# Performance work log

Hardware: AMD Instinct MI355X
Metric: run time of the kernel (lower is better)

Reference implementation:

```python
import jax, jax.numpy as jnp
import numpy as np

B, T, P, D = 8, 512, 2048, 768
TOKEN_HALF = 0.15
PATCH_HALF = 0.03  # small patch boxes


def _make_boxes(key, b, n, half):
    c = jax.random.uniform(key, (b, n, 2), dtype=jnp.float32)
    lo = jnp.clip(c - half, 0.0, 1.0)
    hi = jnp.clip(c + half, 0.0, 1.0)
    return jnp.concatenate([lo, hi], axis=-1)  # (b, n, 4): x0,y0,x1,y1


def setup_inputs() -> dict:
    key = jax.random.key(0)
    k1, k2, k3, k4 = jax.random.split(key, 4)
    patch_feats = jax.random.normal(k1, (B, P, D), dtype=jnp.float32)
    token_boxes = _make_boxes(k2, B, T, TOKEN_HALF)
    patch_boxes = _make_boxes(k3, B, P, PATCH_HALF)
    token_mask = jnp.ones((B, T), dtype=bool)
    scorer_w = jax.random.normal(k4, (D,), dtype=jnp.float32) * 0.02
    scorer_b = jnp.zeros((1,), dtype=jnp.float32)
    return {"patch_feats": patch_feats, "token_boxes": token_boxes,
            "patch_boxes": patch_boxes, "token_mask": token_mask,
            "scorer_w": scorer_w, "scorer_b": scorer_b}


def _patches_in_token_boxes(patch_boxes, tb):
    # patch center containment test: (B,T,P) bool
    cx = 0.5 * (patch_boxes[..., 0] + patch_boxes[..., 2])  # (B,P)
    cy = 0.5 * (patch_boxes[..., 1] + patch_boxes[..., 3])  # (B,P)
    cx = cx[:, None, :]
    cy = cy[:, None, :]
    return ((cx >= tb[..., 0:1]) & (cx <= tb[..., 2:3]) &
            (cy >= tb[..., 1:2]) & (cy <= tb[..., 3:4]))


def reference(patch_feats, token_boxes, patch_boxes, token_mask, scorer_w, scorer_b):
    # normalize token boxes if given in 0..1000 coords (data-dependent, via where)
    tb = token_boxes
    scale = jnp.where(tb.max() > 1.5, jnp.float32(1.0 / 1000.0), jnp.float32(1.0))
    tb = tb * scale

    in_box = _patches_in_token_boxes(patch_boxes, tb)          # (B,T,P)
    in_box = in_box & token_mask[:, :, None]
    region_mask = jnp.any(in_box, axis=-1)                      # (B,T)

    scores = patch_feats @ scorer_w + scorer_b[0]               # (B,P)
    scores = jnp.broadcast_to(scores[:, None, :], in_box.shape)  # (B,T,P)
    scores = jnp.where(in_box, scores, jnp.float32(-10000.0))
    attn = jax.nn.softmax(scores, axis=-1)                      # (B,T,P)

    region_feats = jnp.einsum('btp,bpd->btd', attn, patch_feats)
    region_feats = region_feats * region_mask[..., None].astype(region_feats.dtype)
    return region_feats, region_mask
```

## Files before the change

### kernel.cpp

```cpp
#include <hip/hip_runtime.h>

#define B 8
#define T 512
#define P 2048
#define D 768
#define KDIM P
#define NSPLIT 2
#define KSPLIT (KDIM / NSPLIT)

typedef unsigned short ushort_t;
using short8 = __attribute__((ext_vector_type(8))) short;
using f32x4v = __attribute__((ext_vector_type(4))) float;

#define IDX_SCALE 0
#define IDX_SCORES 64
#define IDX_SCORES2 (64 + B*P)
#define IDX_CX (64 + B*P)
#define IDX_CY (64 + 2*B*P)
#define OFF_ATTN_BYTES 197120
#define OFF_FT_BYTES (OFF_ATTN_BYTES + (size_t)B*T*P*2)
#define OFF_PART_BYTES (OFF_FT_BYTES + (size_t)B*D*P*2)
#define WS_NEED (OFF_PART_BYTES + (size_t)NSPLIT*B*T*D*2)

#define GLD16(gsrc, ldst) \
    __builtin_amdgcn_global_load_lds((const __attribute__((address_space(1))) void*)(gsrc), \
                                     (__attribute__((address_space(3))) void*)(ldst), 16, 0, 0)

#define SCHED_FENCE() __builtin_amdgcn_sched_barrier(0)
#define RAW_BARRIER() do { SCHED_FENCE(); __builtin_amdgcn_s_barrier(); SCHED_FENCE(); } while (0)

__device__ inline ushort_t f2bf(float x) {
    union { float f; unsigned u; } v; v.f = x;
    unsigned r = v.u + 0x7fffu + ((v.u >> 16) & 1u);
    return (ushort_t)(r >> 16);
}

__global__ void k_scale(const float* __restrict__ tboxes, float* __restrict__ ws) {
    __shared__ float red[4];
    int tid = threadIdx.x;
    float m = -1e30f;
    const float4* tb4 = (const float4*)tboxes;
    #pragma unroll
    for (int i = 0; i < 16; ++i) {
        float4 v = tb4[tid + i * 256];
        m = fmaxf(fmaxf(fmaxf(m, v.x), fmaxf(v.y, v.z)), v.w);
    }
    #pragma unroll
    for (int off = 1; off < 64; off <<= 1) m = fmaxf(m, __shfl_xor(m, off));
    if ((tid & 63) == 0) red[tid >> 6] = m;
    __syncthreads();
    if (tid == 0) {
        float mb = fmaxf(fmaxf(red[0], red[1]), fmaxf(red[2], red[3]));
        ws[IDX_SCALE] = (mb > 1.5f) ? (1.0f / 1000.0f) : 1.0f;
    }
}

__global__ __launch_bounds__(256) void k_prep(const float* __restrict__ feats,
        const float* __restrict__ w, float* __restrict__ ws, ushort_t* __restrict__ fT) {
    __shared__ float tile[2][64][65];
    __shared__ float sred[64][17];
    const int t = threadIdx.x;
    const int p0 = blockIdx.x * 64;
    const int z = blockIdx.y;
    const int b = blockIdx.z;
    const float4* f4 = (const float4*)(feats + ((size_t)b * P + p0) * D);
    const float4* w4 = (const float4*)w;
    const int tr = t >> 4, tc = t & 15;
    float sp[4] = {0.f, 0.f, 0.f, 0.f};

    float4 v[4];
    {
        int dt = z * 6;
        #pragma unroll
        for (int i = 0; i < 4; ++i)
            v[i] = f4[(size_t)(tr + 16 * i) * 192 + dt * 16 + tc];
    }
    int cur = 0;
    for (int it = 0; it < 6; ++it) {
        const int dt = z * 6 + it;
        float4 wv = w4[dt * 16 + tc];
        #pragma unroll
        for (int i = 0; i < 4; ++i) {
            int pr = tr + 16 * i;
            sp[i] += v[i].x * wv.x + v[i].y * wv.y + v[i].z * wv.z + v[i].w * wv.w;
            tile[cur][pr][tc * 4 + 0] = v[i].x;
            tile[cur][pr][tc * 4 + 1] = v[i].y;
            tile[cur][pr][tc * 4 + 2] = v[i].z;
            tile[cur][pr][tc * 4 + 3] = v[i].w;
        }
        __syncthreads();
        if (it < 5) {
            int dt2 = dt + 1;
            #pragma unroll
            for (int i = 0; i < 4; ++i)
                v[i] = f4[(size_t)(tr + 16 * i) * 192 + dt2 * 16 + tc];
        }
        #pragma unroll
        for (int pass = 0; pass < 4; ++pass) {
            int idx = pass * 256 + t;
            int dr = idx >> 4;
            int pq = (idx & 15) * 4;
            unsigned u0 = (unsigned)f2bf(tile[cur][pq + 0][dr]) |
                          ((unsigned)f2bf(tile[cur][pq + 1][dr]) << 16);
            unsigned u1 = (unsigned)f2bf(tile[cur][pq + 2][dr]) |
                          ((unsigned)f2bf(tile[cur][pq + 3][dr]) << 16);
            uint2 o; o.x = u0; o.y = u1;
            *(uint2*)&fT[((size_t)b * D + dt * 64 + dr) * P + p0 + pq] = o;
        }
        cur ^= 1;
    }
    #pragma unroll
    for (int i = 0; i < 4; ++i) sred[tr + 16 * i][tc] = sp[i];
    __syncthreads();
    if (t < 64) {
        float s = 0.f;
        #pragma unroll
        for (int c = 0; c < 16; ++c) s += sred[t][c];
        ws[(z ? IDX_SCORES2 : IDX_SCORES) + b * P + p0 + t] = s;
    }
}

__global__ __launch_bounds__(256) void k_attn(const float* __restrict__ tboxes,
        const float* __restrict__ pboxes, const unsigned char* __restrict__ mask8,
        const float* __restrict__ bias, const float* __restrict__ ws,
        ushort_t* __restrict__ attn, float* __restrict__ out) {
    const int wv = threadIdx.x >> 6;
    const int ln = threadIdx.x & 63;
    const int t = blockIdx.x * 4 + wv;
    const int b = blockIdx.y;
    const int row = b * T + t;
    const float scale = ws[IDX_SCALE];
    const float bs = bias[0];
    const float4 tb = ((const float4*)tboxes)[row];
    const float lox = tb.x * scale, loy = tb.y * scale;
    const float hix = tb.z * scale, hiy = tb.w * scale;
    bool storage_u8 = ((mask8[1] | mask8[2] | mask8[3]) != 0);
    bool tmask = storage_u8 ? (mask8[row] != 0) : (((const int*)mask8)[row] != 0);

    const float2* sA = (const float2*)(ws + IDX_SCORES + b * P);
    const float2* sB = (const float2*)(ws + IDX_SCORES2 + b * P);
    const float4* pb4 = (const float4*)(pboxes + (size_t)b * P * 4);
    unsigned* arow32 = (unsigned*)(attn + (size_t)row * P);

    float s0[16], s1[16];
    float m = -1e30f;
    const float NINF = -__builtin_inff();
    #pragma unroll
    for (int r = 0; r < 16; ++r) {
        int q = ln + 64 * r;
        float2 sa = sA[q], sb = sB[q];
        float v0 = sa.x + sb.x + bs;
        float v1 = sa.y + sb.y + bs;
        float4 b0 = pb4[2 * q], b1 = pb4[2 * q + 1];
        float cx0 = 0.5f * (b0.x + b0.z), cy0 = 0.5f * (b0.y + b0.w);
        float cx1 = 0.5f * (b1.x + b1.z), cy1 = 0.5f * (b1.y + b1.w);
        bool i0 = (cx0 >= lox) && (cx0 <= hix) && (cy0 >= loy) && (cy0 <= hiy);
        bool i1 = (cx1 >= lox) && (cx1 <= hix) && (cy1 >= loy) && (cy1 <= hiy);
        s0[r] = i0 ? v0 : NINF;
        s1[r] = i1 ? v1 : NINF;
        m = fmaxf(m, fmaxf(s0[r], s1[r]));
    }
    #pragma unroll
    for (int off = 1; off < 64; off <<= 1) m = fmaxf(m, __shfl_xor(m, off));
    bool any = m > -1e29f;

    if (!any || !tmask) {
        #pragma unroll
        for (int r = 0; r < 16; ++r) arow32[ln + 64 * r] = 0u;
        if (ln == 0) out[(size_t)B * T * D + row] = 0.f;
        return;
    }
    float lsum = 0.f;
    #pragma unroll
    for (int r = 0; r < 16; ++r) {
        s0[r] = __expf(s0[r] - m);
        s1[r] = __expf(s1[r] - m);
        lsum += s0[r] + s1[r];
    }
    #pragma unroll
    for (int off = 1; off < 64; off <<= 1) lsum += __shfl_xor(lsum, off);
    float invl = 1.0f / lsum;
    #pragma unroll
    for (int r = 0; r < 16; ++r) {
        unsigned lo = (unsigned)f2bf(s0[r] * invl);
        unsigned hi = (unsigned)f2bf(s1[r] * invl);
        arow32[ln + 64 * r] = lo | (hi << 16);
    }
    if (ln == 0) out[(size_t)B * T * D + row] = 1.0f;
}

__global__ __launch_bounds__(256, 2) void k_gemm(const ushort_t* __restrict__ attn,
        const ushort_t* __restrict__ fT, ushort_t* __restrict__ partial) {
    __shared__ __align__(16) ushort_t As[2 * 8192];
    __shared__ __align__(16) ushort_t Bs[2 * 8192];
    const int tid = threadIdx.x;
    const int lane = tid & 63, wid = tid >> 6;
    const int wm = wid >> 1, wn = wid & 1;

    const int bid = blockIdx.x;
    const int g = bid & 7;
    const int i6 = bid >> 3;
    const int tq = g & 3;
    const int s = g >> 2;
    const int b = i6 & 7;
    const int n0 = (i6 >> 3) * 128;
    const int t0 = tq * 128;
    const int kbase = s * KSPLIT;

    const ushort_t* Ab = attn + ((size_t)b * T + t0) * P + kbase;
    const ushort_t* Bb = fT + ((size_t)b * D + n0) * P + kbase;

    const int rl8 = lane >> 3;
    const int slot = (lane & 7) ^ rl8;

    f32x4v acc[4][4];
    #pragma unroll
    for (int i = 0; i < 4; ++i)
        #pragma unroll
        for (int j = 0; j < 4; ++j)
            acc[i][j] = (f32x4v){0.f, 0.f, 0.f, 0.f};

    const int lr = lane & 15, hi4 = lane >> 4;

    #define STAGE(buf, kt) do { \
        const ushort_t* a_src = Ab + (size_t)(kt) * 64; \
        const ushort_t* b_src = Bb + (size_t)(kt) * 64; \
        _Pragma("unroll") \
        for (int i = 0; i < 4; ++i) { \
            int c = wid * 4 + i; \
            GLD16(a_src + (size_t)(c * 8 + rl8) * P + slot * 8, &As[(buf) * 8192 + c * 512]); \
        } \
        _Pragma("unroll") \
        for (int i = 0; i < 4; ++i) { \
            int c = wid * 4 + i; \
            GLD16(b_src + (size_t)(c * 8 + rl8) * P + slot * 8, &Bs[(buf) * 8192 + c * 512]); \
        } \
    } while (0)

    #define LDA(row, kslot) (((row) >> 3) * 512 + ((row) & 7) * 64 + (((kslot) ^ ((row) & 7)) * 8))

    #define COMPUTE(buf) do { \
        _Pragma("unroll") \
        for (int ks = 0; ks < 2; ++ks) { \
            short8 a[4], bfr[4]; \
            int kslot = ks * 4 + hi4; \
            _Pragma("unroll") \
            for (int i = 0; i < 4; ++i) \
                a[i] = *(const short8*)&As[(buf) * 8192 + LDA(wm * 64 + i * 16 + lr, kslot)]; \
            _Pragma("unroll") \
            for (int j = 0; j < 4; ++j) \
                bfr[j] = *(const short8*)&Bs[(buf) * 8192 + LDA(wn * 64 + j * 16 + lr, kslot)]; \
            _Pragma("unroll") \
            for (int i = 0; i < 4; ++i) \
                _Pragma("unroll") \
                for (int j = 0; j < 4; ++j) \
                    acc[i][j] = __builtin_amdgcn_mfma_f32_16x16x32_bf16(a[i], bfr[j], acc[i][j], 0, 0, 0); \
        } \
    } while (0)

    STAGE(0, 0);
    int cur = 0;
    for (int kt = 0; kt < KSPLIT / 64 - 1; ++kt) {
        STAGE(cur ^ 1, kt + 1);
        asm volatile("s_waitcnt vmcnt(8)" ::: "memory");
        RAW_BARRIER();
        COMPUTE(cur);
        RAW_BARRIER();
        cur ^= 1;
    }
    asm volatile("s_waitcnt vmcnt(0)" ::: "memory");
    RAW_BARRIER();
    COMPUTE(cur);

    ushort_t* pout = partial + (size_t)s * B * T * D;
    #pragma unroll
    for (int i = 0; i < 4; ++i) {
        #pragma unroll
        for (int j = 0; j < 4; ++j) {
            int trow = t0 + wm * 64 + i * 16 + hi4 * 4;
            int ncol = n0 + wn * 64 + j * 16 + lr;
            #pragma unroll
            for (int q = 0; q < 4; ++q)
                pout[((size_t)(b * T) + trow + q) * D + ncol] = f2bf(acc[i][j][q]);
        }
    }
    #undef STAGE
    #undef LDA
    #undef COMPUTE
}

__global__ __launch_bounds__(256) void k_reduce(const ushort_t* __restrict__ partial,
                                                float* __restrict__ out) {
    const size_t i = (size_t)blockIdx.x * 256 + threadIdx.x;
    const size_t stride = (size_t)(B * T * D) / 8;
    const uint4* p = (const uint4*)partial;
    uint4 a = p[i], b2 = p[i + stride];
    float4 r0, r1;
    r0.x = __uint_as_float(a.x << 16)          + __uint_as_float(b2.x << 16);
    r0.y = __uint_as_float(a.x & 0xffff0000u)  + __uint_as_float(b2.x & 0xffff0000u);
    r0.z = __uint_as_float(a.y << 16)          + __uint_as_float(b2.y << 16);
    r0.w = __uint_as_float(a.y & 0xffff0000u)  + __uint_as_float(b2.y & 0xffff0000u);
    r1.x = __uint_as_float(a.z << 16)          + __uint_as_float(b2.z << 16);
    r1.y = __uint_as_float(a.z & 0xffff0000u)  + __uint_as_float(b2.z & 0xffff0000u);
    r1.z = __uint_as_float(a.w << 16)          + __uint_as_float(b2.w << 16);
    r1.w = __uint_as_float(a.w & 0xffff0000u)  + __uint_as_float(b2.w & 0xffff0000u);
    ((float4*)out)[2 * i]     = r0;
    ((float4*)out)[2 * i + 1] = r1;
}

__global__ __launch_bounds__(256) void k_scores_fb(
        const float* __restrict__ feats, const float* __restrict__ pboxes,
        const float* __restrict__ w, const float* __restrict__ bias,
        float* __restrict__ ws) {
    int row = blockIdx.x * 4 + (threadIdx.x >> 6);
    int lane = threadIdx.x & 63;
    const float* f = feats + (size_t)row * D;
    float acc = 0.f;
    #pragma unroll
    for (int k = 0; k < D / 64; ++k) acc += f[lane + k * 64] * w[lane + k * 64];
    #pragma unroll
    for (int off = 1; off < 64; off <<= 1) acc += __shfl_xor(acc, off);
    if (lane == 0) {
        ws[IDX_SCORES + row] = acc + bias[0];
        ws[IDX_CX + row] = 0.5f * (pboxes[row * 4 + 0] + pboxes[row * 4 + 2]);
        ws[IDX_CY + row] = 0.5f * (pboxes[row * 4 + 1] + pboxes[row * 4 + 3]);
    }
}

__global__ __launch_bounds__(256) void k_main_fb(
        const float* __restrict__ feats, const float* __restrict__ tboxes,
        const unsigned char* __restrict__ mask8,
        const float* __restrict__ ws, float* __restrict__ out) {
    const int t = blockIdx.x, b = blockIdx.y;
    const int tid = threadIdx.x;
    const float scale = ws[IDX_SCALE];
    const float* scores = ws + IDX_SCORES;
    const float* cxs = ws + IDX_CX;
    const float* cys = ws + IDX_CY;
    const int row = b * T + t;
    const float lo_x = tboxes[row * 4 + 0] * scale;
    const float lo_y = tboxes[row * 4 + 1] * scale;
    const float hi_x = tboxes[row * 4 + 2] * scale;
    const float hi_y = tboxes[row * 4 + 3] * scale;
    bool storage_u8 = ((mask8[1] | mask8[2] | mask8[3]) != 0);
    bool tmask = storage_u8 ? (mask8[row] != 0) : (((const int*)mask8)[row] != 0);
    float s[8]; bool ib[8];
    float m = -1e30f;
    #pragma unroll
    for (int j = 0; j < 8; ++j) {
        int p = tid + j * 256;
        float cx = cxs[b * P + p], cy = cys[b * P + p];
        bool in = (cx >= lo_x) && (cx <= hi_x) && (cy >= lo_y) && (cy <= hi_y);
        ib[j] = in;
        s[j] = scores[b * P + p];
        if (in) m = fmaxf(m, s[j]);
    }
    __shared__ float s_red[4];
    #pragma unroll
    for (int off = 1; off < 64; off <<= 1) m = fmaxf(m, __shfl_xor(m, off));
    if ((tid & 63) == 0) s_red[tid >> 6] = m;
    __syncthreads();
    float mb = fmaxf(fmaxf(s_red[0], s_red[1]), fmaxf(s_red[2], s_red[3]));
    bool any = mb > -1e29f;
    const size_t obase = (size_t)row * D;
    if (!any || !tmask) {
        out[obase + tid] = 0.f; out[obase + tid + 256] = 0.f; out[obase + tid + 512] = 0.f;
        if (tid == 0) out[(size_t)B * T * D + row] = 0.f;
        return;
    }
    float w8[8]; int c = 0; float lsum = 0.f;
    #pragma unroll
    for (int j = 0; j < 8; ++j) {
        float wv = ib[j] ? __expf(s[j] - mb) : 0.f;
        w8[j] = wv; lsum += wv;
        if (ib[j]) ++c;
    }
    __shared__ float s_sum[4];
    #pragma unroll
    for (int off = 1; off < 64; off <<= 1) lsum += __shfl_xor(lsum, off);
    if ((tid & 63) == 0) s_sum[tid >> 6] = lsum;
    __syncthreads();
    float l = s_sum[0] + s_sum[1] + s_sum[2] + s_sum[3];
    __shared__ int s_cnt[256];
    s_cnt[tid] = c;
    __syncthreads();
    #pragma unroll
    for (int off = 1; off < 256; off <<= 1) {
        int v = (tid >= off) ? s_cnt[tid - off] : 0;
        __syncthreads();
        s_cnt[tid] += v;
        __syncthreads();
    }
    int excl = s_cnt[tid] - c;
    int nnz = s_cnt[255];
    __shared__ int s_idx[P];
    __shared__ float s_wt[P];
    int o = excl;
    #pragma unroll
    for (int j = 0; j < 8; ++j) {
        if (ib[j]) { s_idx[o] = tid + j * 256; s_wt[o] = w8[j]; ++o; }
    }
    __syncthreads();
    float a0 = 0.f, a1 = 0.f, a2 = 0.f;
    const float* fb = feats + (size_t)b * P * D;
    for (int i = 0; i < nnz; ++i) {
        int p = s_idx[i];
        float wv = s_wt[i];
        const float* fr = fb + (size_t)p * D + tid;
        a0 += wv * fr[0]; a1 += wv * fr[256]; a2 += wv * fr[512];
    }
    float inv = 1.0f / l;
    out[obase + tid] = a0 * inv;
    out[obase + tid + 256] = a1 * inv;
    out[obase + tid + 512] = a2 * inv;
    if (tid == 0) out[(size_t)B * T * D + row] = 1.0f;
}

extern "C" void kernel_launch(void* const* d_in, const int* in_sizes, int n_in,
                              void* d_out, int out_size, void* d_ws, size_t ws_size,
                              hipStream_t stream) {
    const float* feats  = (const float*)d_in[0];
    const float* tboxes = (const float*)d_in[1];
    const float* pboxes = (const float*)d_in[2];
    const unsigned char* tmask = (const unsigned char*)d_in[3];
    const float* w      = (const float*)d_in[4];
    const float* bias   = (const float*)d_in[5];
    float* out = (float*)d_out;
    float* ws  = (float*)d_ws;

    if (ws_size >= WS_NEED) {
        ushort_t* attn = (ushort_t*)((char*)d_ws + OFF_ATTN_BYTES);
        ushort_t* fT   = (ushort_t*)((char*)d_ws + OFF_FT_BYTES);
        ushort_t* part = (ushort_t*)((char*)d_ws + OFF_PART_BYTES);
        k_scale<<<1, 256, 0, stream>>>(tboxes, ws);
        k_prep<<<dim3(P / 64, 2, B), 256, 0, stream>>>(feats, w, ws, fT);
        k_attn<<<dim3(T / 4, B), 256, 0, stream>>>(tboxes, pboxes, tmask, bias, ws, attn, out);
        k_gemm<<<dim3(NSPLIT * B * (T / 128) * (D / 128)), 256, 0, stream>>>(attn, fT, part);
        k_reduce<<<dim3(B * T * D / 8 / 256), 256, 0, stream>>>(part, out);
    } else {
        k_scale<<<1, 256, 0, stream>>>(tboxes, ws);
        k_scores_fb<<<(B * P) / 4, 256, 0, stream>>>(feats, pboxes, w, bias, ws);
        k_main_fb<<<dim3(T, B), 256, 0, stream>>>(feats, tboxes, tmask, ws, out);
    }
}
```

Baseline: 62.62 us.

## Fuse split-K reduction into GEMM via atomic tile counters and fold scale into prep

Removes the separate split-K reduce kernel. Each GEMM block writes its bf16 partial, bumps a per-tile atomic counter, and the second block to finish adds the other partial and writes the fp32 output. The token-box max/scale computation also moves into one block of the prep kernel, where the counters are zeroed too. Together these cut two kernel launches and one full pass over the partial buffer. The cost is fences, an atomic per block, and a data dependency on k_prep running before k_attn reads the scale, which holds given stream order.

New measurement: 146.0 us. 133% more time.

```diff
diff --git a/kernel.cpp b/kernel.cpp
--- a/kernel.cpp
+++ b/kernel.cpp
@@ -20,7 +20,9 @@
 #define OFF_ATTN_BYTES 197120
 #define OFF_FT_BYTES (OFF_ATTN_BYTES + (size_t)B*T*P*2)
 #define OFF_PART_BYTES (OFF_FT_BYTES + (size_t)B*D*P*2)
-#define WS_NEED (OFF_PART_BYTES + (size_t)NSPLIT*B*T*D*2)
+#define OFF_CTR_BYTES (OFF_PART_BYTES + (size_t)NSPLIT*B*T*D*2)
+#define NTILES (B * (T/128) * (D/128))
+#define WS_NEED (OFF_CTR_BYTES + (size_t)NTILES*4)
 
 #define GLD16(gsrc, ldst) \
     __builtin_amdgcn_global_load_lds((const __attribute__((address_space(1))) void*)(gsrc), \
@@ -33,6 +35,9 @@
     union { float f; unsigned u; } v; v.f = x;
     unsigned r = v.u + 0x7fffu + ((v.u >> 16) & 1u);
     return (ushort_t)(r >> 16);
+}
+__device__ inline float bf2f(ushort_t u) {
+    return __uint_as_float(((unsigned)u) << 16);
 }
 
 __global__ void k_scale(const float* __restrict__ tboxes, float* __restrict__ ws) {
@@ -56,13 +61,36 @@
 }
 
 __global__ __launch_bounds__(256) void k_prep(const float* __restrict__ feats,
-        const float* __restrict__ w, float* __restrict__ ws, ushort_t* __restrict__ fT) {
+        const float* __restrict__ w, const float* __restrict__ tboxes,
+        float* __restrict__ ws, ushort_t* __restrict__ fT, int* __restrict__ ctr) {
     __shared__ float tile[2][64][65];
     __shared__ float sred[64][17];
     const int t = threadIdx.x;
     const int p0 = blockIdx.x * 64;
     const int z = blockIdx.y;
     const int b = blockIdx.z;
+
+    if (blockIdx.x == 1 && z == 0 && b == 0 && t < NTILES) ctr[t] = 0;
+    if (blockIdx.x == 0 && z == 0 && b == 0) {
+        __shared__ float red[4];
+        float m = -1e30f;
+        const float4* tb4 = (const float4*)tboxes;
+        #pragma unroll
+        for (int i = 0; i < 16; ++i) {
+            float4 v = tb4[t + i * 256];
+            m = fmaxf(fmaxf(fmaxf(m, v.x), fmaxf(v.y, v.z)), v.w);
+        }
+        #pragma unroll
+        for (int off = 1; off < 64; off <<= 1) m = fmaxf(m, __shfl_xor(m, off));
+        if ((t & 63) == 0) red[t >> 6] = m;
+        __syncthreads();
+        if (t == 0) {
+            float mb = fmaxf(fmaxf(red[0], red[1]), fmaxf(red[2], red[3]));
+            ws[IDX_SCALE] = (mb > 1.5f) ? (1.0f / 1000.0f) : 1.0f;
+        }
+        __syncthreads();
+    }
+
     const float4* f4 = (const float4*)(feats + ((size_t)b * P + p0) * D);
     const float4* w4 = (const float4*)w;
     const int tr = t >> 4, tc = t & 15;
@@ -190,9 +218,11 @@
 }
 
 __global__ __launch_bounds__(256, 2) void k_gemm(const ushort_t* __restrict__ attn,
-        const ushort_t* __restrict__ fT, ushort_t* __restrict__ partial) {
+        const ushort_t* __restrict__ fT, ushort_t* __restrict__ partial,
+        int* __restrict__ ctr, float* __restrict__ out) {
     __shared__ __align__(16) ushort_t As[2 * 8192];
     __shared__ __align__(16) ushort_t Bs[2 * 8192];
+    __shared__ int s_old;
     const int tid = threadIdx.x;
     const int lane = tid & 63, wid = tid >> 6;
     const int wm = wid >> 1, wn = wid & 1;
@@ -206,6 +236,7 @@
     const int n0 = (i6 >> 3) * 128;
     const int t0 = tq * 128;
     const int kbase = s * KSPLIT;
+    const int cid = b * 24 + tq * 6 + (i6 >> 3);
 
     const ushort_t* Ab = attn + ((size_t)b * T + t0) * P + kbase;
     const ushort_t* Bb = fT + ((size_t)b * D + n0) * P + kbase;
@@ -272,7 +303,8 @@
     RAW_BARRIER();
     COMPUTE(cur);
 
-    ushort_t* pout = partial + (size_t)s * B * T * D;
+    ushort_t myb[4][4][4];
+    ushort_t* pown = partial + (size_t)s * B * T * D;
     #pragma unroll
     for (int i = 0; i < 4; ++i) {
         #pragma unroll
@@ -280,32 +312,37 @@
             int trow = t0 + wm * 64 + i * 16 + hi4 * 4;
             int ncol = n0 + wn * 64 + j * 16 + lr;
             #pragma unroll
-            for (int q = 0; q < 4; ++q)
-                pout[((size_t)(b * T) + trow + q) * D + ncol] = f2bf(acc[i][j][q]);
+            for (int q = 0; q < 4; ++q) {
+                ushort_t v = f2bf(acc[i][j][q]);
+                myb[i][j][q] = v;
+                pown[((size_t)(b * T) + trow + q) * D + ncol] = v;
+            }
+        }
+    }
+    __threadfence();
+    __syncthreads();
+    if (tid == 0) s_old = atomicAdd(&ctr[cid], 1);
+    __syncthreads();
+    if (s_old == 1) {
+        __threadfence();
+        const ushort_t* poth = partial + (size_t)(1 - s) * B * T * D;
+        #pragma unroll
+        for (int i = 0; i < 4; ++i) {
+            #pragma unroll
+            for (int j = 0; j < 4; ++j) {
+                int trow = t0 + wm * 64 + i * 16 + hi4 * 4;
+                int ncol = n0 + wn * 64 + j * 16 + lr;
+                #pragma unroll
+                for (int q = 0; q < 4; ++q) {
+                    size_t idx = ((size_t)(b * T) + trow + q) * D + ncol;
+                    out[idx] = bf2f(myb[i][j][q]) + bf2f(poth[idx]);
+                }
+            }
         }
     }
     #undef STAGE
     #undef LDA
     #undef COMPUTE
-}
-
-__global__ __launch_bounds__(256) void k_reduce(const ushort_t* __restrict__ partial,
-                                                float* __restrict__ out) {
-    const size_t i = (size_t)blockIdx.x * 256 + threadIdx.x;
-    const size_t stride = (size_t)(B * T * D) / 8;
-    const uint4* p = (const uint4*)partial;
-    uint4 a = p[i], b2 = p[i + stride];
-    float4 r0, r1;
-    r0.x = __uint_as_float(a.x << 16)          + __uint_as_float(b2.x << 16);
-    r0.y = __uint_as_float(a.x & 0xffff0000u)  + __uint_as_float(b2.x & 0xffff0000u);
-    r0.z = __uint_as_float(a.y << 16)          + __uint_as_float(b2.y << 16);
-    r0.w = __uint_as_float(a.y & 0xffff0000u)  + __uint_as_float(b2.y & 0xffff0000u);
-    r1.x = __uint_as_float(a.z << 16)          + __uint_as_float(b2.z << 16);
-    r1.y = __uint_as_float(a.z & 0xffff0000u)  + __uint_as_float(b2.z & 0xffff0000u);
-    r1.z = __uint_as_float(a.w << 16)          + __uint_as_float(b2.w << 16);
-    r1.w = __uint_as_float(a.w & 0xffff0000u)  + __uint_as_float(b2.w & 0xffff0000u);
-    ((float4*)out)[2 * i]     = r0;
-    ((float4*)out)[2 * i + 1] = r1;
 }
 
 __global__ __launch_bounds__(256) void k_scores_fb(
@@ -432,11 +469,10 @@
         ushort_t* attn = (ushort_t*)((char*)d_ws + OFF_ATTN_BYTES);
         ushort_t* fT   = (ushort_t*)((char*)d_ws + OFF_FT_BYTES);
         ushort_t* part = (ushort_t*)((char*)d_ws + OFF_PART_BYTES);
-        k_scale<<<1, 256, 0, stream>>>(tboxes, ws);
-        k_prep<<<dim3(P / 64, 2, B), 256, 0, stream>>>(feats, w, ws, fT);
+        int* ctr       = (int*)((char*)d_ws + OFF_CTR_BYTES);
+        k_prep<<<dim3(P / 64, 2, B), 256, 0, stream>>>(feats, w, tboxes, ws, fT, ctr);
         k_attn<<<dim3(T / 4, B), 256, 0, stream>>>(tboxes, pboxes, tmask, bias, ws, attn, out);
-        k_gemm<<<dim3(NSPLIT * B * (T / 128) * (D / 128)), 256, 0, stream>>>(attn, fT, part);
-        k_reduce<<<dim3(B * T * D / 8 / 256), 256, 0, stream>>>(part, out);
+        k_gemm<<<dim3(NSPLIT * B * (T / 128) * (D / 128)), 256, 0, stream>>>(attn, fT, part, ctr, out);
     } else {
         k_scale<<<1, 256, 0, stream>>>(tboxes, ws);
         k_scores_fb<<<(B * P) / 4, 256, 0, stream>>>(feats, pboxes, w, bias, ws);
```
